# Optimization experiments

Measured on AMD Instinct MI355X. Metric: run time of the kernel, lower is better.

Reference implementation:

```python
import jax, jax.numpy as jnp
import numpy as np

N = 500_000   # nodes
E = 16_000_000  # edges (avg degree 32)


def setup_inputs() -> dict:
    key = jax.random.key(0)
    ks = jax.random.split(key, 12)
    x = jax.random.normal(ks[0], (N, 1), dtype=jnp.float32)
    edge_index = jax.random.randint(ks[1], (2, E), 0, N, dtype=jnp.int32)
    # GCNConv weights: conv1(1->4), conv2(4->4), conv3(4->2), classifier Linear(2->1)
    def w(k, fin, fout):
        return jax.random.normal(k, (fin, fout), dtype=jnp.float32) / np.sqrt(fin)
    W1, b1 = w(ks[2], 1, 4), jnp.zeros((4,), jnp.float32)
    W2, b2 = w(ks[3], 4, 4), jnp.zeros((4,), jnp.float32)
    W3, b3 = w(ks[4], 4, 2), jnp.zeros((2,), jnp.float32)
    Wc, bc = w(ks[5], 2, 1), jnp.zeros((1,), jnp.float32)
    return {"x": x, "edge_index": edge_index, "W1": W1, "b1": b1,
            "W2": W2, "b2": b2, "W3": W3, "b3": b3, "Wc": Wc, "bc": bc}


def _gcn_conv(h, src, dst, dinv, W, b):
    # PyG GCNConv: out = D^{-1/2}(A+I)D^{-1/2} (h W) + b
    h = h @ W  # [N, Fout], tiny Fout so transform-first is cheapest
    norm = dinv[src] * dinv[dst]          # [E]
    msg = h[src] * norm[:, None]          # [E, Fout]
    agg = jax.ops.segment_sum(msg, dst, num_segments=N)
    # self-loop contribution: norm = dinv[i]^2
    agg = agg + h * (dinv * dinv)[:, None]
    return agg + b


def reference(x, edge_index, W1, b1, W2, b2, W3, b3, Wc, bc):
    src, dst = edge_index[0], edge_index[1]
    # degree including self-loop (count of incoming edges at dst, PyG gcn_norm)
    deg = jax.ops.segment_sum(jnp.ones((E,), jnp.float32), dst, num_segments=N) + 1.0
    dinv = jax.lax.rsqrt(deg)
    h = jnp.tanh(_gcn_conv(x, src, dst, dinv, W1, b1))
    h = jnp.tanh(_gcn_conv(h, src, dst, dinv, W2, b2))
    h = jnp.tanh(_gcn_conv(h, src, dst, dinv, W3, b3))
    out = h @ Wc + bc
    return (out, h)
```

## Files before the change

kernel.cpp:

```cpp
#include <hip/hip_runtime.h>

#define NN   500000
#define NE   16000000
#define NBIN 1954

#define NBUCK   245
#define NWGA    1000
#define CHUNKA4 4000
#define NWGB    2000
#define CHUNKB4 2000
#define CAP     14336

typedef int      vint4   __attribute__((ext_vector_type(4)));
typedef float    vfloat4 __attribute__((ext_vector_type(4)));
typedef float    vfloat2 __attribute__((ext_vector_type(2)));
typedef _Float16 vhalf4  __attribute__((ext_vector_type(4)));
typedef _Float16 vhalf2  __attribute__((ext_vector_type(2)));

__global__ __launch_bounds__(256) void hist_kernel(const int* __restrict__ dst,
                                                   int* __restrict__ wgHist,
                                                   int shift, int nbin, int chunk4) {
    __shared__ int hist[NBIN];
    for (int i = threadIdx.x; i < nbin; i += 256) hist[i] = 0;
    __syncthreads();
    const vint4* d4 = (const vint4*)(dst + (size_t)blockIdx.x * chunk4 * 4);
    for (int i = threadIdx.x; i < chunk4; i += 256) {
        vint4 d = __builtin_nontemporal_load(d4 + i);
        atomicAdd(&hist[d.x >> shift], 1);
        atomicAdd(&hist[d.y >> shift], 1);
        atomicAdd(&hist[d.z >> shift], 1);
        atomicAdd(&hist[d.w >> shift], 1);
    }
    __syncthreads();
    int* row = wgHist + (size_t)blockIdx.x * nbin;
    for (int i = threadIdx.x; i < nbin; i += 256) row[i] = hist[i];
}

__global__ __launch_bounds__(256) void scanbins_kernel(int* __restrict__ wgHist,
                                                       int* __restrict__ binTotal,
                                                       int nwg, int nbin) {
    __shared__ int partials[256];
    int bin = blockIdx.x;
    int t = threadIdx.x;
    int per = (nwg + 255) / 256;
    int w0 = t * per;
    int w1 = w0 + per; if (w1 > nwg) w1 = nwg;
    int s = 0;
    for (int w = w0; w < w1; ++w) s += wgHist[(size_t)w * nbin + bin];
    partials[t] = s;
    __syncthreads();
    if (t == 0) {
        int run = 0;
        for (int i = 0; i < 256; ++i) { int tmp = partials[i]; partials[i] = run; run += tmp; }
        binTotal[bin] = run;
    }
    __syncthreads();
    int off = partials[t];
    for (int w = w0; w < w1; ++w) {
        size_t idx = (size_t)w * nbin + bin;
        int v = wgHist[idx];
        wgHist[idx] = off;
        off += v;
    }
}

__global__ void scantotal_kernel(const int* __restrict__ binTotal, int* __restrict__ binStart,
                                 int nbin) {
    __shared__ int partials[512];
    int t = threadIdx.x;
    int base = t * 4;
    int v[4]; int s = 0;
#pragma unroll
    for (int j = 0; j < 4; ++j) {
        int b = base + j;
        v[j] = (b < nbin) ? binTotal[b] : 0;
        s += v[j];
    }
    partials[t] = s;
    __syncthreads();
    if (t == 0) {
        int run = 0;
        for (int i = 0; i < 512; ++i) { int tmp = partials[i]; partials[i] = run; run += tmp; }
        binStart[nbin] = run;
    }
    __syncthreads();
    int off = partials[t];
#pragma unroll
    for (int j = 0; j < 4; ++j) {
        int b = base + j;
        if (b < nbin) binStart[b] = off;
        off += v[j];
    }
}

__global__ __launch_bounds__(256) void reorder_kernel(const int* __restrict__ src,
                                                      const int* __restrict__ dst,
                                                      const int* __restrict__ wgHist,
                                                      const int* __restrict__ binStart,
                                                      int* __restrict__ outbuf,
                                                      int shift, int nbin, int chunk4) {
    __shared__ int cur[NBIN];
    const int* row = wgHist + (size_t)blockIdx.x * nbin;
    for (int i = threadIdx.x; i < nbin; i += 256) cur[i] = binStart[i] + row[i];
    __syncthreads();
    const int mask = (1 << shift) - 1;
    const vint4* s4 = (const vint4*)(src + (size_t)blockIdx.x * chunk4 * 4);
    const vint4* d4 = (const vint4*)(dst + (size_t)blockIdx.x * chunk4 * 4);
    for (int i = threadIdx.x; i < chunk4; i += 256) {
        vint4 s = __builtin_nontemporal_load(s4 + i);
        vint4 d = __builtin_nontemporal_load(d4 + i);
        int ss[4] = {s.x, s.y, s.z, s.w};
        int dd[4] = {d.x, d.y, d.z, d.w};
#pragma unroll
        for (int k = 0; k < 4; ++k) {
            int pos = atomicAdd(&cur[dd[k] >> shift], 1);
            outbuf[pos] = (ss[k] << shift) | (dd[k] & mask);
        }
    }
}

__global__ __launch_bounds__(1024) void count_kernel(const int* __restrict__ bktStart,
                                                     const int* __restrict__ bucketbuf,
                                                     const float* __restrict__ x,
                                                     float* __restrict__ dinv,
                                                     float* __restrict__ p1,
                                                     int* __restrict__ rowStart) {
    __shared__ int cnt[2048];
    __shared__ int partials[1024];
    int b = blockIdx.x, t = threadIdx.x;
    for (int k = t; k < 2048; k += 1024) cnt[k] = 0;
    __syncthreads();
    int e0 = bktStart[b], e1 = bktStart[b + 1];
    int i = e0 + t;
    for (; i + 3 * 1024 < e1; i += 4 * 1024) {
        int a = bucketbuf[i];
        int c = bucketbuf[i + 1024];
        int d = bucketbuf[i + 2048];
        int e = bucketbuf[i + 3072];
        atomicAdd(&cnt[a & 2047], 1);
        atomicAdd(&cnt[c & 2047], 1);
        atomicAdd(&cnt[d & 2047], 1);
        atomicAdd(&cnt[e & 2047], 1);
    }
    for (; i < e1; i += 1024)
        atomicAdd(&cnt[bucketbuf[i] & 2047], 1);
    __syncthreads();
    int base = t * 2;
    int c0 = cnt[base], c1 = cnt[base + 1];
    partials[t] = c0 + c1;
    __syncthreads();
    if (t == 0) {
        int run = 0;
        for (int k = 0; k < 1024; ++k) { int tmp = partials[k]; partials[k] = run; run += tmp; }
    }
    __syncthreads();
    int off = partials[t];
    int cc[2] = {c0, c1};
#pragma unroll
    for (int j = 0; j < 2; ++j) {
        int k = base + j;
        int node = b * 2048 + k;
        if (node < NN) {
            rowStart[node] = e0 + off;
            float di = rsqrtf((float)cc[j] + 1.0f);
            dinv[node] = di;
            p1[node] = x[node] * di;
        }
        off += cc[j];
    }
    if (b == NBUCK - 1 && t == 0) rowStart[NN] = e1;
}

__global__ __launch_bounds__(1024) void scat2_kernel(const int* __restrict__ bktStart,
                                                     const int* __restrict__ bucketbuf,
                                                     const int* __restrict__ rowStart,
                                                     const float* __restrict__ p1,
                                                     const float* __restrict__ dinv,
                                                     const float* __restrict__ W1,
                                                     const float* __restrict__ b1,
                                                     const float* __restrict__ W2,
                                                     int* __restrict__ edgebuf,
                                                     vhalf4* __restrict__ p2h) {
    __shared__ int   cur[2048];
    __shared__ float acc[2048];
    int b = blockIdx.x, t = threadIdx.x;
    for (int k = t; k < 2048; k += 1024) {
        int node = b * 2048 + k;
        cur[k] = (node < NN) ? rowStart[node] : 0;
        acc[k] = 0.0f;
    }
    __syncthreads();
    int e0 = bktStart[b], e1 = bktStart[b + 1];
    int i = e0 + t;
    for (; i + 3 * 1024 < e1; i += 4 * 1024) {
        int ea = bucketbuf[i];
        int eb = bucketbuf[i + 1024];
        int ec = bucketbuf[i + 2048];
        int ed = bucketbuf[i + 3072];
        int la = ea & 2047, sa = ea >> 11;
        int lb = eb & 2047, sb = eb >> 11;
        int lc = ec & 2047, sc = ec >> 11;
        int ld = ed & 2047, sd = ed >> 11;
        float va = p1[sa];
        float vb = p1[sb];
        float vc = p1[sc];
        float vd = p1[sd];
        int pa = atomicAdd(&cur[la], 1);
        int pb = atomicAdd(&cur[lb], 1);
        int pc = atomicAdd(&cur[lc], 1);
        int pd = atomicAdd(&cur[ld], 1);
        edgebuf[pa] = sa;
        edgebuf[pb] = sb;
        edgebuf[pc] = sc;
        edgebuf[pd] = sd;
        atomicAdd(&acc[la], va);
        atomicAdd(&acc[lb], vb);
        atomicAdd(&acc[lc], vc);
        atomicAdd(&acc[ld], vd);
    }
    for (; i < e1; i += 1024) {
        int e = bucketbuf[i];
        int loc = e & 2047, srcn = e >> 11;
        int pos = atomicAdd(&cur[loc], 1);
        edgebuf[pos] = srcn;
        atomicAdd(&acc[loc], p1[srcn]);
    }
    __syncthreads();
    for (int k = t; k < 2048; k += 1024) {
        int node = b * 2048 + k;
        if (node < NN) {
            float di = dinv[node];
            float tt = di * (acc[k] + p1[node]);
            float h1[4];
#pragma unroll
            for (int f = 0; f < 4; ++f) h1[f] = tanhf(tt * W1[f] + b1[f]);
            vhalf4 g;
            g.x = (_Float16)(di * (h1[0]*W2[0] + h1[1]*W2[4] + h1[2]*W2[8]  + h1[3]*W2[12]));
            g.y = (_Float16)(di * (h1[0]*W2[1] + h1[1]*W2[5] + h1[2]*W2[9]  + h1[3]*W2[13]));
            g.z = (_Float16)(di * (h1[0]*W2[2] + h1[1]*W2[6] + h1[2]*W2[10] + h1[3]*W2[14]));
            g.w = (_Float16)(di * (h1[0]*W2[3] + h1[1]*W2[7] + h1[2]*W2[11] + h1[3]*W2[15]));
            p2h[node] = g;
        }
    }
}

__global__ __launch_bounds__(256) void sortbin_kernel(const int* __restrict__ binStart,
                                                      int* __restrict__ edgebuf,
                                                      const float* __restrict__ x,
                                                      float* __restrict__ dinv,
                                                      float* __restrict__ p1,
                                                      int* __restrict__ rowStart) {
    __shared__ int stage[CAP];
    __shared__ int cnt[256];
    __shared__ int pref[256];
    __shared__ int cur[256];
    int b = blockIdx.x, t = threadIdx.x;
    cnt[t] = 0;
    __syncthreads();
    int e0 = binStart[b], e1 = binStart[b + 1];
    int n = e1 - e0;
    if (n > CAP) n = CAP;
    for (int i = t; i < n; i += 256) {
        int e = edgebuf[e0 + i];
        stage[i] = e;
        atomicAdd(&cnt[e & 255], 1);
    }
    __syncthreads();
    if (t == 0) {
        int run = 0;
        for (int i = 0; i < 256; ++i) { pref[i] = run; run += cnt[i]; }
    }
    __syncthreads();
    cur[t] = pref[t];
    int node = b * 256 + t;
    if (node < NN) {
        rowStart[node] = e0 + pref[t];
        float di = rsqrtf((float)cnt[t] + 1.0f);
        dinv[node] = di;
        p1[node] = x[node] * di;
    }
    if (b == NBIN - 1 && t == 0) rowStart[NN] = binStart[NBIN];
    __syncthreads();
    for (int i = t; i < n; i += 256) {
        int e = stage[i];
        int pos = e0 + atomicAdd(&cur[e & 255], 1);
        edgebuf[pos] = e >> 8;
    }
}

__global__ __launch_bounds__(256) void agg1_kernel(const int* __restrict__ rowStart,
                                                   const int* __restrict__ edgebuf,
                                                   const float* __restrict__ p1,
                                                   const float* __restrict__ dinv,
                                                   const float* __restrict__ W1,
                                                   const float* __restrict__ b1,
                                                   const float* __restrict__ W2,
                                                   vhalf4* __restrict__ p2h) {
    int node = blockIdx.x * blockDim.x + threadIdx.x;
    if (node >= NN) return;
    int r0 = rowStart[node], r1 = rowStart[node + 1];
    float s0 = 0.f, s1 = 0.f, s2 = 0.f, s3 = 0.f;
    float s4 = 0.f, s5 = 0.f, s6 = 0.f, s7 = 0.f;
    int k = r0;
    for (; k + 8 <= r1; k += 8) {
        int a = edgebuf[k],     b = edgebuf[k + 1];
        int c = edgebuf[k + 2], d = edgebuf[k + 3];
        int e = edgebuf[k + 4], f = edgebuf[k + 5];
        int g = edgebuf[k + 6], h = edgebuf[k + 7];
        s0 += p1[a]; s1 += p1[b]; s2 += p1[c]; s3 += p1[d];
        s4 += p1[e]; s5 += p1[f]; s6 += p1[g]; s7 += p1[h];
    }
    for (; k < r1; ++k) s0 += p1[edgebuf[k]];
    float acc = ((s0 + s1) + (s2 + s3)) + ((s4 + s5) + (s6 + s7));
    float di = dinv[node];
    float t = di * (acc + p1[node]);
    float h1[4];
#pragma unroll
    for (int f2 = 0; f2 < 4; ++f2) h1[f2] = tanhf(t * W1[f2] + b1[f2]);
    vhalf4 g;
    g.x = (_Float16)(di * (h1[0]*W2[0] + h1[1]*W2[4] + h1[2]*W2[8]  + h1[3]*W2[12]));
    g.y = (_Float16)(di * (h1[0]*W2[1] + h1[1]*W2[5] + h1[2]*W2[9]  + h1[3]*W2[13]));
    g.z = (_Float16)(di * (h1[0]*W2[2] + h1[1]*W2[6] + h1[2]*W2[10] + h1[3]*W2[14]));
    g.w = (_Float16)(di * (h1[0]*W2[3] + h1[1]*W2[7] + h1[2]*W2[11] + h1[3]*W2[15]));
    p2h[node] = g;
}

__global__ __launch_bounds__(256) void agg2_kernel(const int* __restrict__ rowStart,
                                                   const int* __restrict__ edgebuf,
                                                   const vhalf4* __restrict__ p2h,
                                                   const float* __restrict__ dinv,
                                                   const float* __restrict__ b2,
                                                   const float* __restrict__ W3,
                                                   vhalf2* __restrict__ p3h) {
    int node = blockIdx.x * blockDim.x + threadIdx.x;
    if (node >= NN) return;
    int r0 = rowStart[node], r1 = rowStart[node + 1];
    vfloat4 sA = {0.f, 0.f, 0.f, 0.f};
    vfloat4 sB = {0.f, 0.f, 0.f, 0.f};
    vfloat4 sC = {0.f, 0.f, 0.f, 0.f};
    vfloat4 sD = {0.f, 0.f, 0.f, 0.f};
    int k = r0;
    for (; k + 8 <= r1; k += 8) {
        int a = edgebuf[k],     b = edgebuf[k + 1];
        int c = edgebuf[k + 2], d = edgebuf[k + 3];
        int e = edgebuf[k + 4], f = edgebuf[k + 5];
        int g = edgebuf[k + 6], h = edgebuf[k + 7];
        vhalf4 qa = p2h[a], qb = p2h[b], qc = p2h[c], qd = p2h[d];
        vhalf4 qe = p2h[e], qf = p2h[f], qg = p2h[g], qh = p2h[h];
        sA.x += (float)qa.x + (float)qb.x; sB.x += (float)qc.x + (float)qd.x;
        sA.y += (float)qa.y + (float)qb.y; sB.y += (float)qc.y + (float)qd.y;
        sA.z += (float)qa.z + (float)qb.z; sB.z += (float)qc.z + (float)qd.z;
        sA.w += (float)qa.w + (float)qb.w; sB.w += (float)qc.w + (float)qd.w;
        sC.x += (float)qe.x + (float)qf.x; sD.x += (float)qg.x + (float)qh.x;
        sC.y += (float)qe.y + (float)qf.y; sD.y += (float)qg.y + (float)qh.y;
        sC.z += (float)qe.z + (float)qf.z; sD.z += (float)qg.z + (float)qh.z;
        sC.w += (float)qe.w + (float)qf.w; sD.w += (float)qg.w + (float)qh.w;
    }
    for (; k < r1; ++k) {
        vhalf4 q = p2h[edgebuf[k]];
        sA.x += (float)q.x; sA.y += (float)q.y; sA.z += (float)q.z; sA.w += (float)q.w;
    }
    float di = dinv[node];
    vhalf4 pw = p2h[node];
    float h2[4];
    h2[0] = tanhf(di * (sA.x + sB.x + sC.x + sD.x + (float)pw.x) + b2[0]);
    h2[1] = tanhf(di * (sA.y + sB.y + sC.y + sD.y + (float)pw.y) + b2[1]);
    h2[2] = tanhf(di * (sA.z + sB.z + sC.z + sD.z + (float)pw.z) + b2[2]);
    h2[3] = tanhf(di * (sA.w + sB.w + sC.w + sD.w + (float)pw.w) + b2[3]);
    vhalf2 o;
    o.x = (_Float16)(di * (h2[0]*W3[0] + h2[1]*W3[2] + h2[2]*W3[4] + h2[3]*W3[6]));
    o.y = (_Float16)(di * (h2[0]*W3[1] + h2[1]*W3[3] + h2[2]*W3[5] + h2[3]*W3[7]));
    p3h[node] = o;
}

__global__ __launch_bounds__(256) void agg3_kernel(const int* __restrict__ rowStart,
                                                   const int* __restrict__ edgebuf,
                                                   const vhalf2* __restrict__ p3h,
                                                   const float* __restrict__ dinv,
                                                   const float* __restrict__ b3,
                                                   const float* __restrict__ Wc,
                                                   const float* __restrict__ bc,
                                                   float* __restrict__ out) {
    int node = blockIdx.x * blockDim.x + threadIdx.x;
    if (node >= NN) return;
    int r0 = rowStart[node], r1 = rowStart[node + 1];
    float ax = 0.f, ay = 0.f, bx = 0.f, by = 0.f;
    float cx = 0.f, cy = 0.f, dx = 0.f, dy = 0.f;
    int k = r0;
    for (; k + 8 <= r1; k += 8) {
        int a = edgebuf[k],     b = edgebuf[k + 1];
        int c = edgebuf[k + 2], d = edgebuf[k + 3];
        int e = edgebuf[k + 4], f = edgebuf[k + 5];
        int g = edgebuf[k + 6], h = edgebuf[k + 7];
        vhalf2 qa = p3h[a], qb = p3h[b], qc = p3h[c], qd = p3h[d];
        vhalf2 qe = p3h[e], qf = p3h[f], qg = p3h[g], qh = p3h[h];
        ax += (float)qa.x + (float)qb.x; bx += (float)qc.x + (float)qd.x;
        ay += (float)qa.y + (float)qb.y; by += (float)qc.y + (float)qd.y;
        cx += (float)qe.x + (float)qf.x; dx += (float)qg.x + (float)qh.x;
        cy += (float)qe.y + (float)qf.y; dy += (float)qg.y + (float)qh.y;
    }
    for (; k < r1; ++k) {
        vhalf2 q = p3h[edgebuf[k]];
        ax += (float)q.x; ay += (float)q.y;
    }
    float di = dinv[node];
    vhalf2 pw = p3h[node];
    float h0 = tanhf(di * (ax + bx + cx + dx + (float)pw.x) + b3[0]);
    float h1 = tanhf(di * (ay + by + cy + dy + (float)pw.y) + b3[1]);
    __builtin_nontemporal_store(h0 * Wc[0] + h1 * Wc[1] + bc[0], out + node);
    vfloat2 hh; hh.x = h0; hh.y = h1;
    __builtin_nontemporal_store(hh, (vfloat2*)(out + NN) + node);
}


extern "C" void kernel_launch(void* const* d_in, const int* in_sizes, int n_in,
                              void* d_out, int out_size, void* d_ws, size_t ws_size,
                              hipStream_t stream) {
    const float* x   = (const float*)d_in[0];
    const int*   ei  = (const int*)d_in[1];
    const float* W1  = (const float*)d_in[2];
    const float* b1  = (const float*)d_in[3];
    const float* W2  = (const float*)d_in[4];
    const float* b2  = (const float*)d_in[5];
    const float* W3  = (const float*)d_in[6];
    const float* b3  = (const float*)d_in[7];
    const float* Wc  = (const float*)d_in[8];
    const float* bc  = (const float*)d_in[9];
    float* out = (float*)d_out;
    float* ws  = (float*)d_ws;

    const int* src = ei;
    const int* dst = ei + NE;

    float*  dinv     = ws;
    float*  p1       = ws + (size_t)NN;
    vhalf4* p2h      = (vhalf4*)(ws + 2ull * NN);
    vhalf2* p3h      = (vhalf2*)(ws + 4ull * NN);
    int*    rowStart = (int*)(ws + 5ull * NN);
    int*    tail     = (int*)(ws + 6ull * NN + 1);

    const int B = 256;
    const int aggGrid = (NN + B - 1) / B;

    const size_t needA = (6ull * NN + 1 + (size_t)NWGA * NBUCK + NBUCK + NBUCK + 1
                          + 2ull * NE) * 4ull;

    if (ws_size >= needA) {
        int* wgHist    = tail;
        int* bktTotal  = wgHist + (size_t)NWGA * NBUCK;
        int* bktStart  = bktTotal + NBUCK;
        int* bucketbuf = bktStart + NBUCK + 1;
        int* edgebuf   = bucketbuf + (size_t)NE;

        hipLaunchKernelGGL(hist_kernel, dim3(NWGA), dim3(B), 0, stream,
                           dst, wgHist, 11, NBUCK, CHUNKA4);
        hipLaunchKernelGGL(scanbins_kernel, dim3(NBUCK), dim3(B), 0, stream,
                           wgHist, bktTotal, NWGA, NBUCK);
        hipLaunchKernelGGL(scantotal_kernel, dim3(1), dim3(512), 0, stream,
                           bktTotal, bktStart, NBUCK);
        hipLaunchKernelGGL(reorder_kernel, dim3(NWGA), dim3(B), 0, stream,
                           src, dst, wgHist, bktStart, bucketbuf, 11, NBUCK, CHUNKA4);
        hipLaunchKernelGGL(count_kernel, dim3(NBUCK), dim3(1024), 0, stream,
                           bktStart, bucketbuf, x, dinv, p1, rowStart);
        hipLaunchKernelGGL(scat2_kernel, dim3(NBUCK), dim3(1024), 0, stream,
                           bktStart, bucketbuf, rowStart, p1, dinv, W1, b1, W2,
                           edgebuf, p2h);
        hipLaunchKernelGGL(agg2_kernel, dim3(aggGrid), dim3(B), 0, stream,
                           rowStart, edgebuf, p2h, dinv, b2, W3, p3h);
        hipLaunchKernelGGL(agg3_kernel, dim3(aggGrid), dim3(B), 0, stream,
                           rowStart, edgebuf, p3h, dinv, b3, Wc, bc, out);
    } else {
        int* wgHist   = tail;
        int* binTotal = wgHist + (size_t)NWGB * NBIN;
        int* binStart = binTotal + NBIN;
        int* edgebuf  = binStart + NBIN + 1;

        hipLaunchKernelGGL(hist_kernel, dim3(NWGB), dim3(B), 0, stream,
                           dst, wgHist, 8, NBIN, CHUNKB4);
        hipLaunchKernelGGL(scanbins_kernel, dim3(NBIN), dim3(B), 0, stream,
                           wgHist, binTotal, NWGB, NBIN);
        hipLaunchKernelGGL(scantotal_kernel, dim3(1), dim3(512), 0, stream,
                           binTotal, binStart, NBIN);
        hipLaunchKernelGGL(reorder_kernel, dim3(NWGB), dim3(B), 0, stream,
                           src, dst, wgHist, binStart, edgebuf, 8, NBIN, CHUNKB4);
        hipLaunchKernelGGL(sortbin_kernel, dim3(NBIN), dim3(B), 0, stream,
                           binStart, edgebuf, x, dinv, p1, rowStart);
        hipLaunchKernelGGL(agg1_kernel, dim3(aggGrid), dim3(B), 0, stream,
                           rowStart, edgebuf, p1, dinv, W1, b1, W2, p2h);
        hipLaunchKernelGGL(agg2_kernel, dim3(aggGrid), dim3(B), 0, stream,
                           rowStart, edgebuf, p2h, dinv, b2, W3, p3h);
        hipLaunchKernelGGL(agg3_kernel, dim3(aggGrid), dim3(B), 0, stream,
                           rowStart, edgebuf, p3h, dinv, b3, Wc, bc, out);
    }
}
```

Before: 679.5 us.

## Split scatter kernel into 8 sub-bin workgroups per bucket filtering by node range

Replaces the 245-workgroup, 1024-thread scatter kernel with 1954 workgroups of 256 threads. Each workgroup rescans its whole parent bucket and handles only edges whose destination falls in its 256-node sub-range, which means eight times the bucketbuf reads. In return there are far more workgroups to fill the GPU and less LDS atomic contention per block. A dummy 8704-int shared padding array, written only under an impossible condition, appears intended to cap occupancy per CU.

```diff
diff --git a/kernel.cpp b/kernel.cpp
--- a/kernel.cpp
+++ b/kernel.cpp
@@ -171,76 +171,83 @@
     if (b == NBUCK - 1 && t == 0) rowStart[NN] = e1;
 }
 
-__global__ __launch_bounds__(1024) void scat2_kernel(const int* __restrict__ bktStart,
-                                                     const int* __restrict__ bucketbuf,
-                                                     const int* __restrict__ rowStart,
-                                                     const float* __restrict__ p1,
-                                                     const float* __restrict__ dinv,
-                                                     const float* __restrict__ W1,
-                                                     const float* __restrict__ b1,
-                                                     const float* __restrict__ W2,
-                                                     int* __restrict__ edgebuf,
-                                                     vhalf4* __restrict__ p2h) {
-    __shared__ int   cur[2048];
-    __shared__ float acc[2048];
-    int b = blockIdx.x, t = threadIdx.x;
-    for (int k = t; k < 2048; k += 1024) {
-        int node = b * 2048 + k;
-        cur[k] = (node < NN) ? rowStart[node] : 0;
-        acc[k] = 0.0f;
-    }
-    __syncthreads();
-    int e0 = bktStart[b], e1 = bktStart[b + 1];
+__global__ __launch_bounds__(256) void sortbin2_kernel(const int* __restrict__ bktStart,
+                                                       const int* __restrict__ bucketbuf,
+                                                       const int* __restrict__ rowStart,
+                                                       const float* __restrict__ p1,
+                                                       const float* __restrict__ dinv,
+                                                       const float* __restrict__ W1,
+                                                       const float* __restrict__ b1,
+                                                       const float* __restrict__ W2,
+                                                       int* __restrict__ edgebuf,
+                                                       vhalf4* __restrict__ p2h) {
+    __shared__ int   cur[256];
+    __shared__ float acc[256];
+    __shared__ int   pad[8704];
+    int bin = blockIdx.x;
+    int bucket = bin >> 3, sub = bin & 7;
+    int t = threadIdx.x;
+    int node = bin * 256 + t;
+    cur[t] = (node < NN) ? rowStart[node] : 0;
+    acc[t] = 0.0f;
+    int e0 = bktStart[bucket], e1 = bktStart[bucket + 1];
+    if (e0 == -1) pad[t] = t;
+    __syncthreads();
     int i = e0 + t;
-    for (; i + 3 * 1024 < e1; i += 4 * 1024) {
+    for (; i + 3 * 256 < e1; i += 4 * 256) {
         int ea = bucketbuf[i];
-        int eb = bucketbuf[i + 1024];
-        int ec = bucketbuf[i + 2048];
-        int ed = bucketbuf[i + 3072];
-        int la = ea & 2047, sa = ea >> 11;
-        int lb = eb & 2047, sb = eb >> 11;
-        int lc = ec & 2047, sc = ec >> 11;
-        int ld = ed & 2047, sd = ed >> 11;
-        float va = p1[sa];
-        float vb = p1[sb];
-        float vc = p1[sc];
-        float vd = p1[sd];
-        int pa = atomicAdd(&cur[la], 1);
-        int pb = atomicAdd(&cur[lb], 1);
-        int pc = atomicAdd(&cur[lc], 1);
-        int pd = atomicAdd(&cur[ld], 1);
-        edgebuf[pa] = sa;
-        edgebuf[pb] = sb;
-        edgebuf[pc] = sc;
-        edgebuf[pd] = sd;
-        atomicAdd(&acc[la], va);
-        atomicAdd(&acc[lb], vb);
-        atomicAdd(&acc[lc], vc);
-        atomicAdd(&acc[ld], vd);
-    }
-    for (; i < e1; i += 1024) {
+        int eb = bucketbuf[i + 256];
+        int ec = bucketbuf[i + 512];
+        int ed = bucketbuf[i + 768];
+        int la = ea & 2047, lb = eb & 2047, lc = ec & 2047, ld = ed & 2047;
+        if ((la >> 8) == sub) {
+            int s = ea >> 11;
+            int pos = atomicAdd(&cur[la & 255], 1);
+            edgebuf[pos] = s;
+            atomicAdd(&acc[la & 255], p1[s]);
+        }
+        if ((lb >> 8) == sub) {
+            int s = eb >> 11;
+            int pos = atomicAdd(&cur[lb & 255], 1);
+            edgebuf[pos] = s;
+            atomicAdd(&acc[lb & 255], p1[s]);
+        }
+        if ((lc >> 8) == sub) {
+            int s = ec >> 11;
+            int pos = atomicAdd(&cur[lc & 255], 1);
+            edgebuf[pos] = s;
+            atomicAdd(&acc[lc & 255], p1[s]);
+        }
+        if ((ld >> 8) == sub) {
+            int s = ed >> 11;
+            int pos = atomicAdd(&cur[ld & 255], 1);
+            edgebuf[pos] = s;
+            atomicAdd(&acc[ld & 255], p1[s]);
+        }
+    }
+    for (; i < e1; i += 256) {
         int e = bucketbuf[i];
-        int loc = e & 2047, srcn = e >> 11;
-        int pos = atomicAdd(&cur[loc], 1);
-        edgebuf[pos] = srcn;
-        atomicAdd(&acc[loc], p1[srcn]);
-    }
-    __syncthreads();
-    for (int k = t; k < 2048; k += 1024) {
-        int node = b * 2048 + k;
-        if (node < NN) {
-            float di = dinv[node];
-            float tt = di * (acc[k] + p1[node]);
-            float h1[4];
+        int loc = e & 2047;
+        if ((loc >> 8) == sub) {
+            int s = e >> 11;
+            int pos = atomicAdd(&cur[loc & 255], 1);
+            edgebuf[pos] = s;
+            atomicAdd(&acc[loc & 255], p1[s]);
+        }
+    }
+    __syncthreads();
+    if (node < NN) {
+        float di = dinv[node];
+        float tt = di * (acc[t] + p1[node]);
+        float h1[4];
 #pragma unroll
-            for (int f = 0; f < 4; ++f) h1[f] = tanhf(tt * W1[f] + b1[f]);
-            vhalf4 g;
-            g.x = (_Float16)(di * (h1[0]*W2[0] + h1[1]*W2[4] + h1[2]*W2[8]  + h1[3]*W2[12]));
-            g.y = (_Float16)(di * (h1[0]*W2[1] + h1[1]*W2[5] + h1[2]*W2[9]  + h1[3]*W2[13]));
-            g.z = (_Float16)(di * (h1[0]*W2[2] + h1[1]*W2[6] + h1[2]*W2[10] + h1[3]*W2[14]));
-            g.w = (_Float16)(di * (h1[0]*W2[3] + h1[1]*W2[7] + h1[2]*W2[11] + h1[3]*W2[15]));
-            p2h[node] = g;
-        }
+        for (int f = 0; f < 4; ++f) h1[f] = tanhf(tt * W1[f] + b1[f]);
+        vhalf4 g;
+        g.x = (_Float16)(di * (h1[0]*W2[0] + h1[1]*W2[4] + h1[2]*W2[8]  + h1[3]*W2[12]));
+        g.y = (_Float16)(di * (h1[0]*W2[1] + h1[1]*W2[5] + h1[2]*W2[9]  + h1[3]*W2[13]));
+        g.z = (_Float16)(di * (h1[0]*W2[2] + h1[1]*W2[6] + h1[2]*W2[10] + h1[3]*W2[14]));
+        g.w = (_Float16)(di * (h1[0]*W2[3] + h1[1]*W2[7] + h1[2]*W2[11] + h1[3]*W2[15]));
+        p2h[node] = g;
     }
 }
 
@@ -462,7 +469,7 @@
                            src, dst, wgHist, bktStart, bucketbuf, 11, NBUCK, CHUNKA4);
         hipLaunchKernelGGL(count_kernel, dim3(NBUCK), dim3(1024), 0, stream,
                            bktStart, bucketbuf, x, dinv, p1, rowStart);
-        hipLaunchKernelGGL(scat2_kernel, dim3(NBUCK), dim3(1024), 0, stream,
+        hipLaunchKernelGGL(sortbin2_kernel, dim3(NBIN), dim3(B), 0, stream,
                            bktStart, bucketbuf, rowStart, p1, dinv, W1, b1, W2,
                            edgebuf, p2h);
         hipLaunchKernelGGL(agg2_kernel, dim3(aggGrid), dim3(B), 0, stream,
```

Result: slower. 780.0 us (+14.8%).
